# Optimization experiments

Measured on AMD Instinct MI355X. Metric: run time of the kernel, lower is better.

## Reference

```python
import jax, jax.numpy as jnp
import numpy as np

N_USER = 100000
N_RECIPE = 50000
E = 1000000
H = 128


def setup_inputs() -> dict:
    key = jax.random.key(0)
    ks = jax.random.split(key, 5)
    z_user = jax.random.normal(ks[0], (N_USER, H), dtype=jnp.float32)
    z_recipe = jax.random.normal(ks[1], (N_RECIPE, H), dtype=jnp.float32)
    edge_label_index = jax.random.randint(ks[2], (2, E), 0, N_RECIPE, dtype=jnp.int64)
    W1 = jax.random.normal(ks[3], (2 * H, H), dtype=jnp.float32) * (1.0 / np.sqrt(2 * H))
    b1 = jnp.zeros((H,), dtype=jnp.float32)
    W2 = jax.random.normal(ks[4], (H, 1), dtype=jnp.float32) * (1.0 / np.sqrt(H))
    b2 = jnp.zeros((1,), dtype=jnp.float32)
    return {"z_user": z_user, "z_recipe": z_recipe,
            "edge_label_index": edge_label_index,
            "W1": W1, "b1": b1, "W2": W2, "b2": b2}


def reference(z_user, z_recipe, edge_label_index, W1, b1, W2, b2):
    row, col = edge_label_index[0], edge_label_index[1]
    # gather + concat: [E, 2H]
    z = jnp.concatenate([z_user[row], z_recipe[col]], axis=-1)
    h = jax.nn.relu(z @ W1 + b1)        # [E, H]
    out = h @ W2 + b2                    # [E, 1]
    return out.reshape(-1)
```

## Files before the change

kernel.cpp:

```cpp
#include <hip/hip_runtime.h>
#include <hip/hip_bf16.h>


#define HDIM 128

typedef __attribute__((ext_vector_type(8))) __bf16 bf16x8;
typedef __attribute__((ext_vector_type(16))) float f32x16;

static __device__ __forceinline__ unsigned short bf16_bits(float x) {
  return __builtin_bit_cast(unsigned short, static_cast<__bf16>(x));
}

static __device__ __forceinline__ float bf2f(unsigned short u) {
  return __builtin_bit_cast(float, ((unsigned int)u) << 16);
}

static __device__ __forceinline__ bf16x8 cvt8(float4 a, float4 b) {
  bf16x8 r;
  r[0] = static_cast<__bf16>(a.x);
  r[1] = static_cast<__bf16>(a.y);
  r[2] = static_cast<__bf16>(a.z);
  r[3] = static_cast<__bf16>(a.w);
  r[4] = static_cast<__bf16>(b.x);
  r[5] = static_cast<__bf16>(b.y);
  r[6] = static_cast<__bf16>(b.z);
  r[7] = static_cast<__bf16>(b.w);
  return r;
}

__global__ __launch_bounds__(512, 2) void proj_nodes(
    const float* __restrict__ zu, int NU, const float* __restrict__ zr, int NR,
    const float* __restrict__ W1, unsigned short* __restrict__ Hu,
    unsigned short* __restrict__ Hr) {
  __shared__ unsigned short Bsw[32768];
  const int tid = threadIdx.x;
  {
    const int n = tid & 127;
    const int kh = tid >> 7;
    const int nt = n >> 5;
    const int nl = n & 31;
#pragma unroll 8
    for (int it = 0; it < 64; ++it) {
      const int k = (it << 2) + kh;
      const float w = W1[k * HDIM + n];
      const int kc = k >> 4;
      const int q = (k >> 3) & 1;
      const int j = k & 7;
      const int ln = (q << 5) | nl;
      Bsw[((((kc << 2) + nt) << 6) | ln) * 8 + j] = bf16_bits(w);
    }
  }
  __syncthreads();

  const int lane = tid & 63;
  const int wid = tid >> 6;
  const int m = lane & 31;
  const int half = lane >> 5;
  const int koff = half * 8;
  const int utiles = NU >> 5;
  const int rtiles = (NR + 31) >> 5;
  const int ntiles = utiles + rtiles;
  const int wstride = gridDim.x * 8;

  for (int t = blockIdx.x * 8 + wid; t < ntiles; t += wstride) {
    const bool isU = t < utiles;
    const int base = isU ? (t << 5) : ((t - utiles) << 5);
    const int nmax = isU ? NU : NR;
    const bool full = (base + 32) <= nmax;
    int node = base + m;
    if (node >= nmax) node = nmax - 1;
    const float* src = (isU ? zu : zr) + (size_t)node * HDIM + koff;
    const int kc0 = isU ? 0 : 8;

    f32x16 acc[4];
#pragma unroll
    for (int nt = 0; nt < 4; ++nt) acc[nt] = (f32x16)0.0f;

#pragma unroll
    for (int kcl = 0; kcl < 8; ++kcl) {
      const float4* sa = (const float4*)(src + kcl * 16);
      const bf16x8 a = cvt8(sa[0], sa[1]);
#pragma unroll
      for (int nt = 0; nt < 4; ++nt) {
        const uint4* bp =
            (const uint4*)(Bsw + (((((kc0 + kcl) << 2) + nt) << 6) | lane) * 8);
        const bf16x8 bfr = __builtin_bit_cast(bf16x8, *bp);
        acc[nt] = __builtin_amdgcn_mfma_f32_32x32x16_bf16(a, bfr, acc[nt], 0, 0, 0);
      }
    }

    unsigned short* H = isU ? Hu : Hr;
    if (full) {
#pragma unroll
      for (int nt = 0; nt < 4; ++nt) {
#pragma unroll
        for (int r = 0; r < 16; ++r) {
          const int row = (r & 3) + ((r >> 2) << 3) + (half << 2);
          H[(size_t)(base + row) * HDIM + (nt << 5) + m] = bf16_bits(acc[nt][r]);
        }
      }
    } else {
#pragma unroll
      for (int nt = 0; nt < 4; ++nt) {
#pragma unroll
        for (int r = 0; r < 16; ++r) {
          const int row = (r & 3) + ((r >> 2) << 3) + (half << 2);
          const int nrow = base + row;
          if (nrow < nmax)
            H[(size_t)nrow * HDIM + (nt << 5) + m] = bf16_bits(acc[nt][r]);
        }
      }
    }
  }
}

static __device__ __forceinline__ float dot8(uint4 a, uint4 b,
                                             const float* b1c,
                                             const float* w2c) {
  const unsigned short* pa = (const unsigned short*)&a;
  const unsigned short* pb = (const unsigned short*)&b;
  float s = 0.f;
#pragma unroll
  for (int j = 0; j < 8; ++j) {
    const float h = bf2f(pa[j]) + bf2f(pb[j]) + b1c[j];
    s = fmaf(fmaxf(h, 0.f), w2c[j], s);
  }
  return s;
}

__global__ __launch_bounds__(256, 4) void edge_pass(
    const unsigned short* __restrict__ Hu, const unsigned short* __restrict__ Hr,
    const int* __restrict__ eidx, const float* __restrict__ b1,
    const float* __restrict__ W2, const float* __restrict__ b2,
    float* __restrict__ out, int E) {
  const int tid = threadIdx.x;
  const int lane = tid & 63;
  const int c = lane & 15;
  const int g = lane >> 4;
  const int wid = blockIdx.x * 4 + (tid >> 6);
  const int stride = gridDim.x * 4 * 16;

  float b1c[8], w2c[8];
#pragma unroll
  for (int j = 0; j < 8; ++j) {
    b1c[j] = b1[c * 8 + j];
    w2c[j] = W2[c * 8 + j];
  }
  const float b2v = b2[0];
  const int co = c * 8;

  int e = wid * 16 + g * 4;
  if (e >= E) return;
  int4 iu = *(const int4*)(eidx + e);
  int4 ir = *(const int4*)(eidx + E + e);

  while (true) {
    const int en = e + stride;
    const bool more = en < E;
    const int ep = more ? en : e;

    const uint4 au0 = *(const uint4*)(Hu + (size_t)iu.x * HDIM + co);
    const uint4 ar0 = *(const uint4*)(Hr + (size_t)ir.x * HDIM + co);
    const uint4 au1 = *(const uint4*)(Hu + (size_t)iu.y * HDIM + co);
    const uint4 ar1 = *(const uint4*)(Hr + (size_t)ir.y * HDIM + co);
    const uint4 au2 = *(const uint4*)(Hu + (size_t)iu.z * HDIM + co);
    const uint4 ar2 = *(const uint4*)(Hr + (size_t)ir.z * HDIM + co);
    const uint4 au3 = *(const uint4*)(Hu + (size_t)iu.w * HDIM + co);
    const uint4 ar3 = *(const uint4*)(Hr + (size_t)ir.w * HDIM + co);

    const int4 niu = *(const int4*)(eidx + ep);
    const int4 nir = *(const int4*)(eidx + E + ep);

    float s0 = dot8(au0, ar0, b1c, w2c);
    float s1 = dot8(au1, ar1, b1c, w2c);
    float s2 = dot8(au2, ar2, b1c, w2c);
    float s3 = dot8(au3, ar3, b1c, w2c);
#pragma unroll
    for (int st = 1; st <= 8; st <<= 1) {
      s0 += __shfl_xor(s0, st);
      s1 += __shfl_xor(s1, st);
      s2 += __shfl_xor(s2, st);
      s3 += __shfl_xor(s3, st);
    }
    if (c == 0) {
      float4 o = make_float4(s0 + b2v, s1 + b2v, s2 + b2v, s3 + b2v);
      *(float4*)(out + e) = o;
    }
    if (!more) break;
    e = en;
    iu = niu;
    ir = nir;
  }
}

__global__ __launch_bounds__(256, 2) void edge_decoder_mfma(
    const float* __restrict__ zu, const float* __restrict__ zr,
    const int* __restrict__ eidx, const float* __restrict__ W1,
    const float* __restrict__ b1, const float* __restrict__ W2,
    const float* __restrict__ b2, float* __restrict__ out, int E) {
  __shared__ unsigned short Bsw[32768];
  const int tid = threadIdx.x;
  {
    const int n = tid & 127;
    const int kh = tid >> 7;
    const int nt = n >> 5;
    const int nl = n & 31;
#pragma unroll 8
    for (int it = 0; it < 128; ++it) {
      const int k = 2 * it + kh;
      const float w = W1[k * HDIM + n];
      const int kc = k >> 4;
      const int q = (k >> 3) & 1;
      const int j = k & 7;
      const int ln = (q << 5) | nl;
      Bsw[((((kc << 2) + nt) << 6) | ln) * 8 + j] = bf16_bits(w);
    }
  }
  __syncthreads();

  const int lane = tid & 63;
  const int wid = tid >> 6;
  const int m = lane & 31;
  const int half = lane >> 5;
  const int nsweep = E >> 6;
  const int wstride = gridDim.x * 4;

  float b1v[4], w2v[4];
#pragma unroll
  for (int nt = 0; nt < 4; ++nt) {
    b1v[nt] = b1[nt * 32 + m];
    w2v[nt] = W2[nt * 32 + m];
  }
  const float b2v = b2[0];
  const int koff = half * 8;

  for (int s = blockIdx.x * 4 + wid; s < nsweep; s += wstride) {
    const int e0 = s << 6;
    const int eA = e0 + m;
    const int eB = e0 + 32 + m;
    const float* puA = zu + (size_t)eidx[eA] * HDIM;
    const float* prA = zr + (size_t)eidx[E + eA] * HDIM;
    const float* puB = zu + (size_t)eidx[eB] * HDIM;
    const float* prB = zr + (size_t)eidx[E + eB] * HDIM;

    f32x16 acc[2][4];
#pragma unroll
    for (int mt = 0; mt < 2; ++mt)
#pragma unroll
      for (int nt = 0; nt < 4; ++nt) acc[mt][nt] = (f32x16)0.0f;

#pragma unroll
    for (int kc = 0; kc < 16; ++kc) {
      const float* srcA = (kc < 8) ? (puA + kc * 16 + koff) : (prA + (kc - 8) * 16 + koff);
      const float* srcB = (kc < 8) ? (puB + kc * 16 + koff) : (prB + (kc - 8) * 16 + koff);
      const float4* sa = (const float4*)srcA;
      const float4* sb = (const float4*)srcB;
      const bf16x8 a0 = cvt8(sa[0], sa[1]);
      const bf16x8 a1 = cvt8(sb[0], sb[1]);
#pragma unroll
      for (int nt = 0; nt < 4; ++nt) {
        const uint4* bp = (const uint4*)(Bsw + ((((kc << 2) + nt) << 6) | lane) * 8);
        const bf16x8 bfr = __builtin_bit_cast(bf16x8, *bp);
        acc[0][nt] = __builtin_amdgcn_mfma_f32_32x32x16_bf16(a0, bfr, acc[0][nt], 0, 0, 0);
        acc[1][nt] = __builtin_amdgcn_mfma_f32_32x32x16_bf16(a1, bfr, acc[1][nt], 0, 0, 0);
      }
    }

    float p0[16], p1[16];
#pragma unroll
    for (int r = 0; r < 16; ++r) { p0[r] = 0.f; p1[r] = 0.f; }
#pragma unroll
    for (int nt = 0; nt < 4; ++nt) {
#pragma unroll
      for (int r = 0; r < 16; ++r) {
        float h0 = fmaxf(acc[0][nt][r] + b1v[nt], 0.f);
        float h1 = fmaxf(acc[1][nt][r] + b1v[nt], 0.f);
        p0[r] = fmaf(h0, w2v[nt], p0[r]);
        p1[r] = fmaf(h1, w2v[nt], p1[r]);
      }
    }
#pragma unroll
    for (int st = 1; st <= 16; st <<= 1) {
#pragma unroll
      for (int r = 0; r < 16; ++r) {
        p0[r] += __shfl_xor(p0[r], st);
        p1[r] += __shfl_xor(p1[r], st);
      }
    }
    const int sel = lane & 15;
    const int mtw = (lane >> 4) & 1;
    float val = 0.f;
#pragma unroll
    for (int r = 0; r < 16; ++r) {
      const float cand = mtw ? p1[r] : p0[r];
      val = (sel == r) ? cand : val;
    }
    const int mrow = (sel & 3) + ((sel >> 2) << 3) + (half << 2);
    out[e0 + (mtw << 5) + mrow] = val + b2v;
  }
}

extern "C" void kernel_launch(void* const* d_in, const int* in_sizes, int n_in,
                              void* d_out, int out_size, void* d_ws,
                              size_t ws_size, hipStream_t stream) {
  const float* zu = (const float*)d_in[0];
  const float* zr = (const float*)d_in[1];
  const int* eidx = (const int*)d_in[2];
  const float* W1 = (const float*)d_in[3];
  const float* b1 = (const float*)d_in[4];
  const float* W2 = (const float*)d_in[5];
  const float* b2 = (const float*)d_in[6];
  float* out = (float*)d_out;
  const int nu = in_sizes[0];
  const int nr = in_sizes[1];
  const int E = in_sizes[2] / 2;
  const int NU = nu / HDIM, NR = nr / HDIM;

  const size_t need = (size_t)(nu + nr) * sizeof(unsigned short);
  if (ws_size >= need && (E % 16) == 0) {
    unsigned short* Hu = (unsigned short*)d_ws;
    unsigned short* Hr = Hu + (size_t)nu;
    const int ntiles = (NU >> 5) + ((NR + 31) >> 5);
    const int pblocks = (ntiles + 7) / 8;
    hipLaunchKernelGGL(proj_nodes, dim3(pblocks), dim3(512), 0, stream,
                       zu, NU, zr, NR, W1, Hu, Hr);
    hipLaunchKernelGGL(edge_pass, dim3(2048), dim3(256), 0, stream,
                       Hu, Hr, eidx, b1, W2, b2, out, E);
  } else {
    hipLaunchKernelGGL(edge_decoder_mfma, dim3(512), dim3(256), 0, stream,
                       zu, zr, eidx, W1, b1, W2, b2, out, E);
  }
}
```

Measured before the change: 197.6 us.

## Split projection blocks by node type to halve LDS and raise occupancy

Each proj_nodes block now handles only user or only recipe nodes, so it stages just its half of W1 in LDS (32KB instead of 64KB). This lets launch bounds ask for 4 blocks per CU and replaces the grid-stride loop with one tile per wave. The edge pass drops its software-prefetch of the next indices in favour of a plain strided loop and is launched with 3x more blocks, relying on more waves in flight to hide gather latency. The cost is more block launches and repeated W1 staging per block.

```diff
diff --git a/kernel.cpp b/kernel.cpp
--- a/kernel.cpp
+++ b/kernel.cpp
@@ -28,21 +28,23 @@
   return r;
 }
 
-__global__ __launch_bounds__(512, 2) void proj_nodes(
+__global__ __launch_bounds__(512, 4) void proj_nodes(
     const float* __restrict__ zu, int NU, const float* __restrict__ zr, int NR,
     const float* __restrict__ W1, unsigned short* __restrict__ Hu,
-    unsigned short* __restrict__ Hr) {
-  __shared__ unsigned short Bsw[32768];
+    unsigned short* __restrict__ Hr, int UB) {
+  __shared__ unsigned short Bsw[16384];
   const int tid = threadIdx.x;
+  const bool isU = (int)blockIdx.x < UB;
+  const int kbase = isU ? 0 : HDIM;
   {
     const int n = tid & 127;
     const int kh = tid >> 7;
     const int nt = n >> 5;
     const int nl = n & 31;
 #pragma unroll 8
-    for (int it = 0; it < 64; ++it) {
+    for (int it = 0; it < 32; ++it) {
       const int k = (it << 2) + kh;
-      const float w = W1[k * HDIM + n];
+      const float w = W1[(kbase + k) * HDIM + n];
       const int kc = k >> 4;
       const int q = (k >> 3) & 1;
       const int j = k & 7;
@@ -57,58 +59,54 @@
   const int m = lane & 31;
   const int half = lane >> 5;
   const int koff = half * 8;
-  const int utiles = NU >> 5;
-  const int rtiles = (NR + 31) >> 5;
-  const int ntiles = utiles + rtiles;
-  const int wstride = gridDim.x * 8;
-
-  for (int t = blockIdx.x * 8 + wid; t < ntiles; t += wstride) {
-    const bool isU = t < utiles;
-    const int base = isU ? (t << 5) : ((t - utiles) << 5);
-    const int nmax = isU ? NU : NR;
-    const bool full = (base + 32) <= nmax;
-    int node = base + m;
-    if (node >= nmax) node = nmax - 1;
-    const float* src = (isU ? zu : zr) + (size_t)node * HDIM + koff;
-    const int kc0 = isU ? 0 : 8;
-
-    f32x16 acc[4];
-#pragma unroll
-    for (int nt = 0; nt < 4; ++nt) acc[nt] = (f32x16)0.0f;
-
-#pragma unroll
-    for (int kcl = 0; kcl < 8; ++kcl) {
-      const float4* sa = (const float4*)(src + kcl * 16);
-      const bf16x8 a = cvt8(sa[0], sa[1]);
-#pragma unroll
-      for (int nt = 0; nt < 4; ++nt) {
-        const uint4* bp =
-            (const uint4*)(Bsw + (((((kc0 + kcl) << 2) + nt) << 6) | lane) * 8);
-        const bf16x8 bfr = __builtin_bit_cast(bf16x8, *bp);
-        acc[nt] = __builtin_amdgcn_mfma_f32_32x32x16_bf16(a, bfr, acc[nt], 0, 0, 0);
-      }
-    }
-
-    unsigned short* H = isU ? Hu : Hr;
-    if (full) {
-#pragma unroll
-      for (int nt = 0; nt < 4; ++nt) {
-#pragma unroll
-        for (int r = 0; r < 16; ++r) {
-          const int row = (r & 3) + ((r >> 2) << 3) + (half << 2);
-          H[(size_t)(base + row) * HDIM + (nt << 5) + m] = bf16_bits(acc[nt][r]);
-        }
-      }
-    } else {
-#pragma unroll
-      for (int nt = 0; nt < 4; ++nt) {
-#pragma unroll
-        for (int r = 0; r < 16; ++r) {
-          const int row = (r & 3) + ((r >> 2) << 3) + (half << 2);
-          const int nrow = base + row;
-          if (nrow < nmax)
-            H[(size_t)nrow * HDIM + (nt << 5) + m] = bf16_bits(acc[nt][r]);
-        }
+
+  const int t = (isU ? (int)blockIdx.x : (int)blockIdx.x - UB) * 8 + wid;
+  const int ntile = isU ? (NU + 31) >> 5 : (NR + 31) >> 5;
+  if (t >= ntile) return;
+
+  const int nmax = isU ? NU : NR;
+  const int base = t << 5;
+  const bool full = (base + 32) <= nmax;
+  int node = base + m;
+  if (node >= nmax) node = nmax - 1;
+  const float* src = (isU ? zu : zr) + (size_t)node * HDIM + koff;
+
+  f32x16 acc[4];
+#pragma unroll
+  for (int nt = 0; nt < 4; ++nt) acc[nt] = (f32x16)0.0f;
+
+#pragma unroll
+  for (int kcl = 0; kcl < 8; ++kcl) {
+    const float4* sa = (const float4*)(src + kcl * 16);
+    const bf16x8 a = cvt8(sa[0], sa[1]);
+#pragma unroll
+    for (int nt = 0; nt < 4; ++nt) {
+      const uint4* bp =
+          (const uint4*)(Bsw + ((((kcl << 2) + nt) << 6) | lane) * 8);
+      const bf16x8 bfr = __builtin_bit_cast(bf16x8, *bp);
+      acc[nt] = __builtin_amdgcn_mfma_f32_32x32x16_bf16(a, bfr, acc[nt], 0, 0, 0);
+    }
+  }
+
+  unsigned short* H = isU ? Hu : Hr;
+  if (full) {
+#pragma unroll
+    for (int nt = 0; nt < 4; ++nt) {
+#pragma unroll
+      for (int r = 0; r < 16; ++r) {
+        const int row = (r & 3) + ((r >> 2) << 3) + (half << 2);
+        H[(size_t)(base + row) * HDIM + (nt << 5) + m] = bf16_bits(acc[nt][r]);
+      }
+    }
+  } else {
+#pragma unroll
+    for (int nt = 0; nt < 4; ++nt) {
+#pragma unroll
+      for (int r = 0; r < 16; ++r) {
+        const int row = (r & 3) + ((r >> 2) << 3) + (half << 2);
+        const int nrow = base + row;
+        if (nrow < nmax)
+          H[(size_t)nrow * HDIM + (nt << 5) + m] = bf16_bits(acc[nt][r]);
       }
     }
   }
@@ -149,15 +147,9 @@
   const float b2v = b2[0];
   const int co = c * 8;
 
-  int e = wid * 16 + g * 4;
-  if (e >= E) return;
-  int4 iu = *(const int4*)(eidx + e);
-  int4 ir = *(const int4*)(eidx + E + e);
-
-  while (true) {
-    const int en = e + stride;
-    const bool more = en < E;
-    const int ep = more ? en : e;
+  for (int e = wid * 16 + g * 4; e < E; e += stride) {
+    const int4 iu = *(const int4*)(eidx + e);
+    const int4 ir = *(const int4*)(eidx + E + e);
 
     const uint4 au0 = *(const uint4*)(Hu + (size_t)iu.x * HDIM + co);
     const uint4 ar0 = *(const uint4*)(Hr + (size_t)ir.x * HDIM + co);
@@ -168,9 +160,6 @@
     const uint4 au3 = *(const uint4*)(Hu + (size_t)iu.w * HDIM + co);
     const uint4 ar3 = *(const uint4*)(Hr + (size_t)ir.w * HDIM + co);
 
-    const int4 niu = *(const int4*)(eidx + ep);
-    const int4 nir = *(const int4*)(eidx + E + ep);
-
     float s0 = dot8(au0, ar0, b1c, w2c);
     float s1 = dot8(au1, ar1, b1c, w2c);
     float s2 = dot8(au2, ar2, b1c, w2c);
@@ -186,10 +175,6 @@
       float4 o = make_float4(s0 + b2v, s1 + b2v, s2 + b2v, s3 + b2v);
       *(float4*)(out + e) = o;
     }
-    if (!more) break;
-    e = en;
-    iu = niu;
-    ir = nir;
   }
 }
 
@@ -320,11 +305,13 @@
   if (ws_size >= need && (E % 16) == 0) {
     unsigned short* Hu = (unsigned short*)d_ws;
     unsigned short* Hr = Hu + (size_t)nu;
-    const int ntiles = (NU >> 5) + ((NR + 31) >> 5);
-    const int pblocks = (ntiles + 7) / 8;
-    hipLaunchKernelGGL(proj_nodes, dim3(pblocks), dim3(512), 0, stream,
-                       zu, NU, zr, NR, W1, Hu, Hr);
-    hipLaunchKernelGGL(edge_pass, dim3(2048), dim3(256), 0, stream,
+    const int utiles = (NU + 31) >> 5;
+    const int rtiles = (NR + 31) >> 5;
+    const int UB = (utiles + 7) / 8;
+    const int RB = (rtiles + 7) / 8;
+    hipLaunchKernelGGL(proj_nodes, dim3(UB + RB), dim3(512), 0, stream,
+                       zu, NU, zr, NR, W1, Hu, Hr, UB);
+    hipLaunchKernelGGL(edge_pass, dim3(6144), dim3(256), 0, stream,
                        Hu, Hr, eidx, b1, W2, b2, out, E);
   } else {
     hipLaunchKernelGGL(edge_decoder_mfma, dim3(512), dim3(256), 0, stream,
```

Result: no change. 196.4 us (-0.6%).
